# Performance work log

Measured on AMD Instinct MI355X. Metric: run time of the kernel, lower is better.

The kernel has to match this reference:

```python
import jax, jax.numpy as jnp
import numpy as np

N = 100_000       # nodes
E = 1_600_000     # edges (avg degree 16)
F_IN = 10         # num_node_features
H = 128           # hidden_dim
L = 3             # num_layers
G = 256           # number of graphs in the batch
C = 25            # num_classes
BN_EPS = 1e-5


def setup_inputs() -> dict:
    key = jax.random.key(0)
    ks = jax.random.split(key, 10)
    s = 0.05
    x = jax.random.normal(ks[0], (N, F_IN), dtype=jnp.float32)
    edge_index = jax.random.randint(ks[1], (2, E), 0, N, dtype=jnp.int32)
    batch = jnp.sort(jax.random.randint(ks[2], (N,), 0, G, dtype=jnp.int32))
    return {
        "x": x,
        "edge_index": edge_index,
        "batch": batch,
        "Wp": jax.random.normal(ks[3], (F_IN, H), dtype=jnp.float32) * s,
        "bp": jnp.zeros((H,), jnp.float32),
        "Wc": jax.random.normal(ks[4], (L, H, H), dtype=jnp.float32) * s,
        "bc": jnp.zeros((L, H), jnp.float32),
        "bn_gamma": jnp.ones((L, H), jnp.float32),
        "bn_beta": jnp.zeros((L, H), jnp.float32),
        "bn_mean": jax.random.normal(ks[5], (L, H), dtype=jnp.float32) * 0.1,
        "bn_var": jax.random.uniform(ks[6], (L, H), minval=0.5, maxval=1.5, dtype=jnp.float32),
        "W1": jax.random.normal(ks[7], (2 * H, H), dtype=jnp.float32) * s,
        "b1": jnp.zeros((H,), jnp.float32),
        "W2": jax.random.normal(ks[8], (H, C), dtype=jnp.float32) * s,
        "b2": jnp.zeros((C,), jnp.float32),
    }


def reference(x, edge_index, batch, Wp, bp, Wc, bc, bn_gamma, bn_beta,
              bn_mean, bn_var, W1, b1, W2, b2):
    n = x.shape[0]
    # GCNConv: add self loops, symmetric degree normalization (eval semantics:
    # batchnorm uses running stats, dropout is identity).
    loop = jnp.arange(n, dtype=edge_index.dtype)
    rows = jnp.concatenate([edge_index[0], loop])  # target / aggregation index
    cols = jnp.concatenate([edge_index[1], loop])  # source / gather index
    deg = jax.ops.segment_sum(jnp.ones_like(rows, dtype=x.dtype), rows, num_segments=n)
    dinv = jax.lax.rsqrt(deg)  # deg >= 1 thanks to self loops
    norm = dinv[rows] * dinv[cols]  # [E+N]

    h = jax.nn.relu(x @ Wp + bp)
    for i in range(L):
        hw = h @ Wc[i]                                   # [N, H]
        msg = hw[cols] * norm[:, None]                   # gather + scale
        agg = jax.ops.segment_sum(msg, rows, num_segments=n) + bc[i]
        bn = (agg - bn_mean[i]) * jax.lax.rsqrt(bn_var[i] + BN_EPS) * bn_gamma[i] + bn_beta[i]
        h = jax.nn.relu(bn)

    counts = jax.ops.segment_sum(jnp.ones((n,), h.dtype), batch, num_segments=G)
    x_mean = jax.ops.segment_sum(h, batch, num_segments=G) / jnp.maximum(counts, 1.0)[:, None]
    x_max = jax.ops.segment_max(h, batch, num_segments=G)
    x_max = jnp.where(counts[:, None] > 0, x_max, 0.0)   # guard empty graphs
    g = jnp.concatenate([x_mean, x_max], axis=1)          # [G, 2H]
    return jax.nn.relu(g @ W1 + b1) @ W2 + b2             # [G, C]
```

## Files before the change

### kernel.cpp

```cpp
#include <hip/hip_runtime.h>

#define N_NODES   100000
#define N_EDGES   1600000
#define F_IN      10
#define HD        128
#define N_LAYERS  3
#define N_GRAPHS  256
#define N_CLASSES 25
#define BN_EPS    1e-5f
#define POOL_TILE 64
#define LDS_PITCH 152
#define CPITCH    136

#define NBUCK     196
#define SCAT_TILE 4096
#define BUCK_CAP  16384
#define PREPW_BLKS ((N_LAYERS*HD*HD)/256)

typedef __attribute__((ext_vector_type(8))) short bf8;
typedef __attribute__((ext_vector_type(4))) float f32x4;

static __device__ __forceinline__ unsigned short f2bf(float f){
    unsigned u = __float_as_uint(f);
    unsigned r = (u + 0x7fffu + ((u >> 16) & 1u)) >> 16;
    return (unsigned short)r;
}
static __device__ __forceinline__ float bflo(unsigned u){ return __uint_as_float(u << 16); }
static __device__ __forceinline__ float bfhi(unsigned u){ return __uint_as_float(u & 0xffff0000u); }
static __device__ __forceinline__ unsigned packbf(float a, float b){
    return (unsigned)f2bf(a) | ((unsigned)f2bf(b) << 16);
}


__global__ __launch_bounds__(256) void k_hist(const int* __restrict__ rows,
        int* __restrict__ gcount, int e){
    __shared__ int lhist[NBUCK];
    int t = threadIdx.x;
    if (t < NBUCK) lhist[t] = 0;
    __syncthreads();
    int i0 = blockIdx.x*SCAT_TILE + t;
    #pragma unroll
    for (int k = 0; k < 16; k++){
        int i = i0 + k*256;
        if (i < e) atomicAdd(&lhist[rows[i] >> 9], 1);
    }
    __syncthreads();
    if (t < NBUCK && lhist[t] > 0) atomicAdd(&gcount[t], lhist[t]);
}

__global__ void k_scanb(const int* __restrict__ gcount, int* __restrict__ base,
        int* __restrict__ cursor, int* __restrict__ rowptr, int e, int n){
    __shared__ int s[256];
    int t = threadIdx.x;
    int v = (t < NBUCK) ? gcount[t] : 0;
    s[t] = v;
    __syncthreads();
    for (int d = 1; d < 256; d <<= 1){
        int tv = (t >= d) ? s[t-d] : 0;
        __syncthreads();
        s[t] += tv;
        __syncthreads();
    }
    if (t < NBUCK){ base[t] = s[t] - v; cursor[t] = s[t] - v; }
    if (t == 0){ base[NBUCK] = e; rowptr[n] = e; }
}

__global__ __launch_bounds__(256) void k_scatter(const int* __restrict__ rows,
        const int* __restrict__ cols, int* __restrict__ cursor,
        unsigned* __restrict__ ebuf, int e){
    __shared__ int lbase[NBUCK];
    __shared__ int lcur[NBUCK];
    __shared__ int gbase[NBUCK];
    __shared__ int sbuf[256];
    __shared__ unsigned sedge[SCAT_TILE];
    __shared__ unsigned char sbuck[SCAT_TILE];
    int t = threadIdx.x;
    int i0 = blockIdx.x*SCAT_TILE + t;
    int r[16], c[16];
    if (t < NBUCK) lcur[t] = 0;
    __syncthreads();
    #pragma unroll
    for (int k = 0; k < 16; k++){
        int i = i0 + k*256;
        if (i < e){
            r[k] = rows[i]; c[k] = cols[i];
            atomicAdd(&lcur[r[k] >> 9], 1);
        } else r[k] = -1;
    }
    __syncthreads();
    int myc = (t < NBUCK) ? lcur[t] : 0;
    sbuf[t] = myc;
    __syncthreads();
    for (int d = 1; d < 256; d <<= 1){
        int tv = (t >= d) ? sbuf[t-d] : 0;
        __syncthreads();
        sbuf[t] += tv;
        __syncthreads();
    }
    if (t < NBUCK){
        lbase[t] = sbuf[t] - myc;
        lcur[t]  = sbuf[t] - myc;
        if (myc > 0) gbase[t] = atomicAdd(&cursor[t], myc);
    }
    __syncthreads();
    #pragma unroll
    for (int k = 0; k < 16; k++){
        if (r[k] >= 0){
            int bk = r[k] >> 9;
            int off = atomicAdd(&lcur[bk], 1);
            sedge[off] = ((unsigned)(r[k] & 511) << 17) | (unsigned)c[k];
            sbuck[off] = (unsigned char)bk;
        }
    }
    __syncthreads();
    int tot = sbuf[255];
    for (int i = t; i < tot; i += 256){
        int bk = sbuck[i];
        ebuf[gbase[bk] + (i - lbase[bk])] = sedge[i];
    }
}

__global__ __launch_bounds__(512) void k_build(const unsigned* __restrict__ ebuf,
        const int* __restrict__ base, int* __restrict__ rowptr,
        float* __restrict__ dinv, int* __restrict__ colidx, int n){
    __shared__ int hist[512];
    __shared__ int cur[512];
    __shared__ int colstage[BUCK_CAP];
    int b = blockIdx.x;
    int s = base[b], e = base[b+1];
    int cnt = e - s;
    int row0 = b << 9;
    int nrows = min(512, n - row0);
    int t = threadIdx.x;
    hist[t] = 0;
    __syncthreads();
    for (int i = t; i < cnt; i += 512)
        atomicAdd(&hist[ebuf[s + i] >> 17], 1);
    __syncthreads();
    int myc = hist[t];
    cur[t] = myc;
    __syncthreads();
    for (int d = 1; d < 512; d <<= 1){
        int tv = (t >= d) ? cur[t-d] : 0;
        __syncthreads();
        cur[t] += tv;
        __syncthreads();
    }
    int excl = cur[t] - myc;
    if (t < nrows){
        rowptr[row0 + t] = s + excl;
        dinv[row0 + t] = rsqrtf((float)(myc + 1));
    }
    cur[t] = excl;
    __syncthreads();
    for (int i = t; i < cnt; i += 512){
        unsigned v = ebuf[s + i];
        int off = atomicAdd(&cur[v >> 17], 1);
        colstage[off] = (int)(v & 0x1ffffu);
    }
    __syncthreads();
    for (int i = t; i < cnt; i += 512)
        colidx[s + i] = colstage[i];
}

__global__ void k_prep(const float* __restrict__ Wc, unsigned short* __restrict__ WT,
                       const float* __restrict__ x, const float* __restrict__ Wp,
                       const float* __restrict__ bp, unsigned* __restrict__ hbf, int n){
    __shared__ float sW[F_IN*HD];
    __shared__ float sb[HD];
    if (blockIdx.x < PREPW_BLKS){
        int i = blockIdx.x*256 + threadIdx.x;
        int l = i >> 14;
        int r = (i >> 7) & 127;
        int c = i & 127;
        WT[(l << 14) + c*HD + r] = f2bf(Wc[i]);
        return;
    }
    int bid = blockIdx.x - PREPW_BLKS;
    for (int t = threadIdx.x; t < F_IN*HD; t += 256) sW[t] = Wp[t];
    if (threadIdx.x < HD) sb[threadIdx.x] = bp[threadIdx.x];
    __syncthreads();
    int j  = threadIdx.x & 63;
    int ln = threadIdx.x >> 6;
    for (int n0 = bid*4 + ln; n0 < n; n0 += 1024*4){
        float a0 = sb[2*j], a1 = sb[2*j+1];
        #pragma unroll
        for (int k = 0; k < F_IN; k++){
            float xv = x[(size_t)n0*F_IN + k];
            a0 += xv * sW[k*HD + 2*j];
            a1 += xv * sW[k*HD + 2*j+1];
        }
        hbf[(size_t)n0*64 + j] = packbf(fmaxf(a0, 0.f), fmaxf(a1, 0.f));
    }
}

__global__ __launch_bounds__(256) void k_gemm(const unsigned short* __restrict__ hbf,
        const unsigned short* __restrict__ WT, const float* __restrict__ dinv,
        unsigned short* __restrict__ hw, int n){
    extern __shared__ char smem[];
    unsigned short* As = (unsigned short*)smem;
    unsigned short* Bs = As + 128*LDS_PITCH;
    int tid = threadIdx.x;
    int row0 = blockIdx.x * 128;

    const uint4* h4 = (const uint4*)hbf;
    const uint4* w4 = (const uint4*)WT;
    #pragma unroll
    for (int q = tid; q < 2048; q += 256){
        int r = q >> 4, c = q & 15;
        uint4 v = make_uint4(0u,0u,0u,0u);
        if (row0 + r < n) v = h4[(size_t)(row0 + r)*16 + c];
        *(uint4*)&As[r*LDS_PITCH + c*8] = v;
        *(uint4*)&Bs[r*LDS_PITCH + c*8] = w4[r*16 + c];
    }
    __syncthreads();

    int w = tid >> 6, lane = tid & 63;
    int l15 = lane & 15, quad = lane >> 4;
    f32x4 acc[2][8];
    #pragma unroll
    for (int rt = 0; rt < 2; rt++)
        #pragma unroll
        for (int ct = 0; ct < 8; ct++) acc[rt][ct] = (f32x4){0.f,0.f,0.f,0.f};

    int arow = w*32 + l15;
    #pragma unroll
    for (int kc = 0; kc < 4; kc++){
        int ko = kc*32 + quad*8;
        bf8 a0 = *(const bf8*)&As[arow*LDS_PITCH + ko];
        bf8 a1 = *(const bf8*)&As[(arow+16)*LDS_PITCH + ko];
        #pragma unroll
        for (int ct = 0; ct < 8; ct++){
            bf8 b = *(const bf8*)&Bs[(ct*16 + l15)*LDS_PITCH + ko];
            acc[0][ct] = __builtin_amdgcn_mfma_f32_16x16x32_bf16(a0, b, acc[0][ct], 0, 0, 0);
            acc[1][ct] = __builtin_amdgcn_mfma_f32_16x16x32_bf16(a1, b, acc[1][ct], 0, 0, 0);
        }
    }
    __syncthreads();

    unsigned short* CS = As;
    #pragma unroll
    for (int rt = 0; rt < 2; rt++){
        #pragma unroll
        for (int reg = 0; reg < 4; reg++){
            int rloc = w*32 + rt*16 + quad*4 + reg;
            int grow = row0 + rloc;
            float dv = (grow < n) ? dinv[grow] : 0.f;
            #pragma unroll
            for (int ct = 0; ct < 8; ct++)
                CS[rloc*CPITCH + ct*16 + l15] = f2bf(acc[rt][ct][reg] * dv);
        }
    }
    __syncthreads();

    #pragma unroll
    for (int q = tid; q < 2048; q += 256){
        int r = q >> 4, c = q & 15;
        if (row0 + r < n)
            *(uint4*)&hw[(size_t)(row0 + r)*HD + c*8] = *(const uint4*)&CS[r*CPITCH + c*8];
    }
}

__global__ __launch_bounds__(256) void k_agg(const unsigned* __restrict__ hw4,
        const int* __restrict__ rowptr, const int* __restrict__ colidx,
        const float* __restrict__ dinv, const float* __restrict__ bc,
        const float* __restrict__ bmean, const float* __restrict__ bvar,
        const float* __restrict__ bgamma, const float* __restrict__ bbeta,
        unsigned* __restrict__ houtb, int n){
    int node = blockIdx.x*4 + (threadIdx.x >> 6);
    int lane = threadIdx.x & 63;
    if (node >= n) return;
    unsigned self = hw4[(size_t)node*64 + lane];
    float ax = bflo(self), ay = bfhi(self);
    float bx = 0.f, by = 0.f;
    int s = rowptr[node], e = rowptr[node+1];
    int t = s;
    for (; t + 8 <= e; t += 8){
        int c0 = colidx[t],   c1 = colidx[t+1];
        int c2 = colidx[t+2], c3 = colidx[t+3];
        int c4 = colidx[t+4], c5 = colidx[t+5];
        int c6 = colidx[t+6], c7 = colidx[t+7];
        unsigned v0 = hw4[(size_t)c0*64 + lane];
        unsigned v1 = hw4[(size_t)c1*64 + lane];
        unsigned v2 = hw4[(size_t)c2*64 + lane];
        unsigned v3 = hw4[(size_t)c3*64 + lane];
        unsigned v4 = hw4[(size_t)c4*64 + lane];
        unsigned v5 = hw4[(size_t)c5*64 + lane];
        unsigned v6 = hw4[(size_t)c6*64 + lane];
        unsigned v7 = hw4[(size_t)c7*64 + lane];
        ax += bflo(v0); ay += bfhi(v0);
        bx += bflo(v1); by += bfhi(v1);
        ax += bflo(v2); ay += bfhi(v2);
        bx += bflo(v3); by += bfhi(v3);
        ax += bflo(v4); ay += bfhi(v4);
        bx += bflo(v5); by += bfhi(v5);
        ax += bflo(v6); ay += bfhi(v6);
        bx += bflo(v7); by += bfhi(v7);
    }
    for (; t + 4 <= e; t += 4){
        int c0 = colidx[t],   c1 = colidx[t+1];
        int c2 = colidx[t+2], c3 = colidx[t+3];
        unsigned v0 = hw4[(size_t)c0*64 + lane];
        unsigned v1 = hw4[(size_t)c1*64 + lane];
        unsigned v2 = hw4[(size_t)c2*64 + lane];
        unsigned v3 = hw4[(size_t)c3*64 + lane];
        ax += bflo(v0); ay += bfhi(v0);
        bx += bflo(v1); by += bfhi(v1);
        ax += bflo(v2); ay += bfhi(v2);
        bx += bflo(v3); by += bfhi(v3);
    }
    for (; t < e; t++){
        unsigned v = hw4[(size_t)colidx[t]*64 + lane];
        ax += bflo(v); ay += bfhi(v);
    }
    ax += bx; ay += by;
    float dv = dinv[node];
    float2 cb  = ((const float2*)bc)[lane];
    float2 cm  = ((const float2*)bmean)[lane];
    float2 cv  = ((const float2*)bvar)[lane];
    float2 cg  = ((const float2*)bgamma)[lane];
    float2 cbe = ((const float2*)bbeta)[lane];
    float rx = (ax*dv + cb.x - cm.x) * rsqrtf(cv.x + BN_EPS) * cg.x + cbe.x;
    float ry = (ay*dv + cb.y - cm.y) * rsqrtf(cv.y + BN_EPS) * cg.y + cbe.y;
    rx = fmaxf(rx, 0.f); ry = fmaxf(ry, 0.f);
    houtb[(size_t)node*64 + lane] = packbf(rx, ry);
}

__global__ void k_pool(const unsigned* __restrict__ hb, const int* __restrict__ batch,
        float* __restrict__ gsum, int* __restrict__ gmax, int n){
    int q = threadIdx.x;
    int start = blockIdx.x * POOL_TILE;
    int end = min(start + POOL_TILE, n);
    if (start >= end) return;
    int cur = batch[start];
    float s0 = 0.f, s1 = 0.f, m0 = 0.f, m1 = 0.f;
    for (int i = start; i < end; i++){
        int b = batch[i];
        unsigned v = hb[(size_t)i*64 + q];
        float v0 = bflo(v), v1 = bfhi(v);
        if (b != cur){
            atomicAdd(&gsum[cur*HD + 2*q],     s0);
            atomicAdd(&gsum[cur*HD + 2*q + 1], s1);
            atomicMax(&gmax[cur*HD + 2*q],     __float_as_int(m0));
            atomicMax(&gmax[cur*HD + 2*q + 1], __float_as_int(m1));
            s0 = s1 = m0 = m1 = 0.f; cur = b;
        }
        s0 += v0; s1 += v1;
        m0 = fmaxf(m0, v0); m1 = fmaxf(m1, v1);
    }
    atomicAdd(&gsum[cur*HD + 2*q],     s0);
    atomicAdd(&gsum[cur*HD + 2*q + 1], s1);
    atomicMax(&gmax[cur*HD + 2*q],     __float_as_int(m0));
    atomicMax(&gmax[cur*HD + 2*q + 1], __float_as_int(m1));
}

__global__ void k_head(const float* __restrict__ gsum, const int* __restrict__ gmax,
        const int* __restrict__ batch, const float* __restrict__ W1,
        const float* __restrict__ b1, const float* __restrict__ W2,
        const float* __restrict__ b2, float* __restrict__ out, int n){
    __shared__ float gv[2*HD];
    __shared__ float hid[HD];
    __shared__ int bound[2];
    int g = blockIdx.x, j = threadIdx.x;
    if (j < 2){
        int target = g + j;
        int lo = 0, hi = n;
        while (lo < hi){ int mid = (lo + hi) >> 1; if (batch[mid] < target) lo = mid + 1; else hi = mid; }
        bound[j] = lo;
    }
    __syncthreads();
    float denom = (float)max(bound[1] - bound[0], 1);
    gv[j]    = gsum[g*HD+j] / denom;
    gv[HD+j] = __int_as_float(gmax[g*HD+j]);
    __syncthreads();
    float acc = b1[j];
    #pragma unroll 8
    for (int k = 0; k < 2*HD; k++) acc += gv[k]*W1[k*HD + j];
    hid[j] = fmaxf(acc, 0.f);
    __syncthreads();
    if (j < N_CLASSES){
        float o = b2[j];
        #pragma unroll 4
        for (int k = 0; k < HD; k++) o += hid[k]*W2[k*N_CLASSES + j];
        out[g*N_CLASSES + j] = o;
    }
}

extern "C" void kernel_launch(void* const* d_in, const int* in_sizes, int n_in,
                              void* d_out, int out_size, void* d_ws, size_t ws_size,
                              hipStream_t stream){
    const float* x   = (const float*)d_in[0];
    const int*  eidx = (const int*)d_in[1];
    const int* batch = (const int*)d_in[2];
    const float* Wp  = (const float*)d_in[3];
    const float* bp  = (const float*)d_in[4];
    const float* Wc  = (const float*)d_in[5];
    const float* bc  = (const float*)d_in[6];
    const float* bng = (const float*)d_in[7];
    const float* bnb = (const float*)d_in[8];
    const float* bnm = (const float*)d_in[9];
    const float* bnv = (const float*)d_in[10];
    const float* W1  = (const float*)d_in[11];
    const float* b1  = (const float*)d_in[12];
    const float* W2  = (const float*)d_in[13];
    const float* b2  = (const float*)d_in[14];
    float* out = (float*)d_out;

    char* ws = (char*)d_ws;
    size_t off = 0;
    unsigned short* h_bf  = (unsigned short*)(ws + off); off += (size_t)N_NODES*HD*2;
    unsigned short* hw_bf = (unsigned short*)(ws + off); off += (size_t)N_NODES*HD*2;
    unsigned short* WT = (unsigned short*)(ws + off); off += (size_t)N_LAYERS*HD*HD*2;
    float* dinv   = (float*)(ws + off); off += (size_t)N_NODES*4;
    int*   rowptr = (int*)  (ws + off); off += (size_t)(N_NODES+16)*4;
    int*   colidx = (int*)  (ws + off); off += (size_t)N_EDGES*4;
    unsigned* ebuf= (unsigned*)(ws + off); off += (size_t)N_EDGES*4;
    int*   bbase  = (int*)  (ws + off); off += 1024;
    int*   bcur   = (int*)  (ws + off); off += 1024;
    int*   gcount = (int*)  (ws + off); off += 1024;
    float* gsum   = (float*)(ws + off); off += (size_t)N_GRAPHS*HD*4;
    int*   gmax   = (int*)  (ws + off); off += (size_t)N_GRAPHS*HD*4;

    const int* rows = eidx;
    const int* cols = eidx + N_EDGES;

    hipMemsetAsync(gcount, 0, 1024 + (size_t)(N_GRAPHS*HD*2)*4, stream);

    int nsb = (N_EDGES + SCAT_TILE - 1)/SCAT_TILE;
    k_hist   <<<nsb, 256, 0, stream>>>(rows, gcount, N_EDGES);
    k_scanb  <<<1, 256, 0, stream>>>(gcount, bbase, bcur, rowptr, N_EDGES, N_NODES);
    k_scatter<<<nsb, 256, 0, stream>>>(rows, cols, bcur, ebuf, N_EDGES);
    k_build  <<<NBUCK, 512, 0, stream>>>(ebuf, bbase, rowptr, dinv, colidx, N_NODES);

    k_prep<<<PREPW_BLKS + 1024, 256, 0, stream>>>(Wc, WT, x, Wp, bp, (unsigned*)h_bf, N_NODES);

    int ntiles = (N_NODES + 127)/128;
    size_t shmem = (size_t)(2*128*LDS_PITCH)*2;
    for (int l = 0; l < N_LAYERS; l++){
        k_gemm<<<ntiles, 256, shmem, stream>>>(h_bf, WT + (size_t)l*HD*HD, dinv, hw_bf, N_NODES);
        k_agg<<<(N_NODES+3)/4, 256, 0, stream>>>((const unsigned*)hw_bf, rowptr, colidx, dinv,
            bc + l*HD, bnm + l*HD, bnv + l*HD, bng + l*HD, bnb + l*HD,
            (unsigned*)h_bf, N_NODES);
    }

    k_pool<<<(N_NODES+POOL_TILE-1)/POOL_TILE, 64, 0, stream>>>((const unsigned*)h_bf, batch, gsum, gmax, N_NODES);
    k_head<<<N_GRAPHS, 128, 0, stream>>>(gsum, gmax, batch, W1, b1, W2, b2, out, N_NODES);
}
```

Before: 439.5 us.

## Fuse aggregation with next-layer GEMM and pooling, merge CSR build kernels

Each layer's neighbor aggregation and batchnorm now feeds the next layer's bf16 MFMA GEMM through LDS in one kernel (64-row tiles). The input projection is fused into the first GEMM and mean/max pooling into the last aggregation. The separate bucket-scan kernel is removed by redoing the scan redundantly in the scatter and build blocks, and the weight transpose is merged into the histogram kernel. This cuts launches and the write and re-read of the intermediate h tensor. The cost is smaller GEMM tiles and aggregation work serialized per wave within a tile.

```diff
diff --git a/kernel.cpp b/kernel.cpp
--- a/kernel.cpp
+++ b/kernel.cpp
@@ -8,14 +8,13 @@
 #define N_GRAPHS  256
 #define N_CLASSES 25
 #define BN_EPS    1e-5f
-#define POOL_TILE 64
-#define LDS_PITCH 152
-#define CPITCH    136
+#define APITCH    136
 
 #define NBUCK     196
 #define SCAT_TILE 4096
 #define BUCK_CAP  16384
 #define PREPW_BLKS ((N_LAYERS*HD*HD)/256)
+#define NTILE     ((N_NODES + 63)/64)
 
 typedef __attribute__((ext_vector_type(8))) short bf8;
 typedef __attribute__((ext_vector_type(4))) float f32x4;
@@ -31,14 +30,23 @@
     return (unsigned)f2bf(a) | ((unsigned)f2bf(b) << 16);
 }
 
-
-__global__ __launch_bounds__(256) void k_hist(const int* __restrict__ rows,
+__global__ __launch_bounds__(256) void k_pre(const float* __restrict__ Wc,
+        unsigned short* __restrict__ WT, const int* __restrict__ rows,
         int* __restrict__ gcount, int e){
     __shared__ int lhist[NBUCK];
     int t = threadIdx.x;
+    if (blockIdx.x < PREPW_BLKS){
+        int i = blockIdx.x*256 + t;
+        int l = i >> 14;
+        int r = (i >> 7) & 127;
+        int c = i & 127;
+        WT[(l << 14) + c*HD + r] = f2bf(Wc[i]);
+        return;
+    }
+    int bid = blockIdx.x - PREPW_BLKS;
     if (t < NBUCK) lhist[t] = 0;
     __syncthreads();
-    int i0 = blockIdx.x*SCAT_TILE + t;
+    int i0 = bid*SCAT_TILE + t;
     #pragma unroll
     for (int k = 0; k < 16; k++){
         int i = i0 + k*256;
@@ -48,26 +56,9 @@
     if (t < NBUCK && lhist[t] > 0) atomicAdd(&gcount[t], lhist[t]);
 }
 
-__global__ void k_scanb(const int* __restrict__ gcount, int* __restrict__ base,
-        int* __restrict__ cursor, int* __restrict__ rowptr, int e, int n){
-    __shared__ int s[256];
-    int t = threadIdx.x;
-    int v = (t < NBUCK) ? gcount[t] : 0;
-    s[t] = v;
-    __syncthreads();
-    for (int d = 1; d < 256; d <<= 1){
-        int tv = (t >= d) ? s[t-d] : 0;
-        __syncthreads();
-        s[t] += tv;
-        __syncthreads();
-    }
-    if (t < NBUCK){ base[t] = s[t] - v; cursor[t] = s[t] - v; }
-    if (t == 0){ base[NBUCK] = e; rowptr[n] = e; }
-}
-
 __global__ __launch_bounds__(256) void k_scatter(const int* __restrict__ rows,
-        const int* __restrict__ cols, int* __restrict__ cursor,
-        unsigned* __restrict__ ebuf, int e){
+        const int* __restrict__ cols, const int* __restrict__ gcount,
+        int* __restrict__ gcur, unsigned* __restrict__ ebuf, int e){
     __shared__ int lbase[NBUCK];
     __shared__ int lcur[NBUCK];
     __shared__ int gbase[NBUCK];
@@ -75,6 +66,17 @@
     __shared__ unsigned sedge[SCAT_TILE];
     __shared__ unsigned char sbuck[SCAT_TILE];
     int t = threadIdx.x;
+    int gval = (t < NBUCK) ? gcount[t] : 0;
+    sbuf[t] = gval;
+    __syncthreads();
+    for (int d = 1; d < 256; d <<= 1){
+        int tv = (t >= d) ? sbuf[t-d] : 0;
+        __syncthreads();
+        sbuf[t] += tv;
+        __syncthreads();
+    }
+    int bucket_base = sbuf[t] - gval;
+    __syncthreads();
     int i0 = blockIdx.x*SCAT_TILE + t;
     int r[16], c[16];
     if (t < NBUCK) lcur[t] = 0;
@@ -100,7 +102,7 @@
     if (t < NBUCK){
         lbase[t] = sbuf[t] - myc;
         lcur[t]  = sbuf[t] - myc;
-        if (myc > 0) gbase[t] = atomicAdd(&cursor[t], myc);
+        if (myc > 0) gbase[t] = bucket_base + atomicAdd(&gcur[t], myc);
     }
     __syncthreads();
     #pragma unroll
@@ -121,17 +123,29 @@
 }
 
 __global__ __launch_bounds__(512) void k_build(const unsigned* __restrict__ ebuf,
-        const int* __restrict__ base, int* __restrict__ rowptr,
-        float* __restrict__ dinv, int* __restrict__ colidx, int n){
+        const int* __restrict__ gcount, int* __restrict__ rowptr,
+        float* __restrict__ dinv, int* __restrict__ colidx, int n, int etot){
     __shared__ int hist[512];
     __shared__ int cur[512];
     __shared__ int colstage[BUCK_CAP];
+    __shared__ int sscan[256];
+    int t = threadIdx.x;
+    int gval = (t < NBUCK) ? gcount[t] : 0;
+    if (t < 256) sscan[t] = gval;
+    __syncthreads();
+    for (int d = 1; d < 256; d <<= 1){
+        int tv = (t < 256 && t >= d) ? sscan[t-d] : 0;
+        __syncthreads();
+        if (t < 256) sscan[t] += tv;
+        __syncthreads();
+    }
     int b = blockIdx.x;
-    int s = base[b], e = base[b+1];
-    int cnt = e - s;
+    int e_ = sscan[b];
+    int s  = e_ - gcount[b];
+    int cnt = e_ - s;
     int row0 = b << 9;
     int nrows = min(512, n - row0);
-    int t = threadIdx.x;
+    if (b == 0 && t == 0) rowptr[n] = etot;
     hist[t] = 0;
     __syncthreads();
     for (int i = t; i < cnt; i += 512)
@@ -163,114 +177,60 @@
         colidx[s + i] = colstage[i];
 }
 
-__global__ void k_prep(const float* __restrict__ Wc, unsigned short* __restrict__ WT,
-                       const float* __restrict__ x, const float* __restrict__ Wp,
-                       const float* __restrict__ bp, unsigned* __restrict__ hbf, int n){
-    __shared__ float sW[F_IN*HD];
-    __shared__ float sb[HD];
-    if (blockIdx.x < PREPW_BLKS){
-        int i = blockIdx.x*256 + threadIdx.x;
-        int l = i >> 14;
-        int r = (i >> 7) & 127;
-        int c = i & 127;
-        WT[(l << 14) + c*HD + r] = f2bf(Wc[i]);
-        return;
-    }
-    int bid = blockIdx.x - PREPW_BLKS;
-    for (int t = threadIdx.x; t < F_IN*HD; t += 256) sW[t] = Wp[t];
-    if (threadIdx.x < HD) sb[threadIdx.x] = bp[threadIdx.x];
-    __syncthreads();
-    int j  = threadIdx.x & 63;
-    int ln = threadIdx.x >> 6;
-    for (int n0 = bid*4 + ln; n0 < n; n0 += 1024*4){
-        float a0 = sb[2*j], a1 = sb[2*j+1];
-        #pragma unroll
-        for (int k = 0; k < F_IN; k++){
-            float xv = x[(size_t)n0*F_IN + k];
-            a0 += xv * sW[k*HD + 2*j];
-            a1 += xv * sW[k*HD + 2*j+1];
-        }
-        hbf[(size_t)n0*64 + j] = packbf(fmaxf(a0, 0.f), fmaxf(a1, 0.f));
-    }
-}
-
-__global__ __launch_bounds__(256) void k_gemm(const unsigned short* __restrict__ hbf,
+static __device__ __forceinline__ void gemm_tile(unsigned short* As, unsigned short* Bs,
         const unsigned short* __restrict__ WT, const float* __restrict__ dinv,
-        unsigned short* __restrict__ hw, int n){
-    extern __shared__ char smem[];
-    unsigned short* As = (unsigned short*)smem;
-    unsigned short* Bs = As + 128*LDS_PITCH;
-    int tid = threadIdx.x;
-    int row0 = blockIdx.x * 128;
-
-    const uint4* h4 = (const uint4*)hbf;
+        unsigned short* __restrict__ hw, int row0, int n, int tid){
     const uint4* w4 = (const uint4*)WT;
     #pragma unroll
     for (int q = tid; q < 2048; q += 256){
         int r = q >> 4, c = q & 15;
-        uint4 v = make_uint4(0u,0u,0u,0u);
-        if (row0 + r < n) v = h4[(size_t)(row0 + r)*16 + c];
-        *(uint4*)&As[r*LDS_PITCH + c*8] = v;
-        *(uint4*)&Bs[r*LDS_PITCH + c*8] = w4[r*16 + c];
+        *(uint4*)&Bs[r*APITCH + c*8] = w4[r*16 + c];
     }
     __syncthreads();
 
     int w = tid >> 6, lane = tid & 63;
     int l15 = lane & 15, quad = lane >> 4;
-    f32x4 acc[2][8];
-    #pragma unroll
-    for (int rt = 0; rt < 2; rt++)
-        #pragma unroll
-        for (int ct = 0; ct < 8; ct++) acc[rt][ct] = (f32x4){0.f,0.f,0.f,0.f};
-
-    int arow = w*32 + l15;
+    f32x4 acc[8];
+    #pragma unroll
+    for (int ct = 0; ct < 8; ct++) acc[ct] = (f32x4){0.f,0.f,0.f,0.f};
+
+    int arow = w*16 + l15;
     #pragma unroll
     for (int kc = 0; kc < 4; kc++){
         int ko = kc*32 + quad*8;
-        bf8 a0 = *(const bf8*)&As[arow*LDS_PITCH + ko];
-        bf8 a1 = *(const bf8*)&As[(arow+16)*LDS_PITCH + ko];
+        bf8 a = *(const bf8*)&As[arow*APITCH + ko];
         #pragma unroll
         for (int ct = 0; ct < 8; ct++){
-            bf8 b = *(const bf8*)&Bs[(ct*16 + l15)*LDS_PITCH + ko];
-            acc[0][ct] = __builtin_amdgcn_mfma_f32_16x16x32_bf16(a0, b, acc[0][ct], 0, 0, 0);
-            acc[1][ct] = __builtin_amdgcn_mfma_f32_16x16x32_bf16(a1, b, acc[1][ct], 0, 0, 0);
+            bf8 b = *(const bf8*)&Bs[(ct*16 + l15)*APITCH + ko];
+            acc[ct] = __builtin_amdgcn_mfma_f32_16x16x32_bf16(a, b, acc[ct], 0, 0, 0);
         }
     }
     __syncthreads();
 
-    unsigned short* CS = As;
-    #pragma unroll
-    for (int rt = 0; rt < 2; rt++){
+    #pragma unroll
+    for (int reg = 0; reg < 4; reg++){
+        int rloc = w*16 + quad*4 + reg;
+        int grow = row0 + rloc;
+        float dv = (grow < n) ? dinv[grow] : 0.f;
         #pragma unroll
-        for (int reg = 0; reg < 4; reg++){
-            int rloc = w*32 + rt*16 + quad*4 + reg;
-            int grow = row0 + rloc;
-            float dv = (grow < n) ? dinv[grow] : 0.f;
-            #pragma unroll
-            for (int ct = 0; ct < 8; ct++)
-                CS[rloc*CPITCH + ct*16 + l15] = f2bf(acc[rt][ct][reg] * dv);
-        }
-    }
-    __syncthreads();
-
-    #pragma unroll
-    for (int q = tid; q < 2048; q += 256){
+        for (int ct = 0; ct < 8; ct++)
+            As[rloc*APITCH + ct*16 + l15] = f2bf(acc[ct][reg] * dv);
+    }
+    __syncthreads();
+
+    #pragma unroll
+    for (int q = tid; q < 1024; q += 256){
         int r = q >> 4, c = q & 15;
         if (row0 + r < n)
-            *(uint4*)&hw[(size_t)(row0 + r)*HD + c*8] = *(const uint4*)&CS[r*CPITCH + c*8];
-    }
-}
-
-__global__ __launch_bounds__(256) void k_agg(const unsigned* __restrict__ hw4,
+            *(uint4*)&hw[(size_t)(row0 + r)*HD + c*8] = *(const uint4*)&As[r*APITCH + c*8];
+    }
+}
+
+static __device__ __forceinline__ unsigned agg_node(const unsigned* __restrict__ hwp,
         const int* __restrict__ rowptr, const int* __restrict__ colidx,
-        const float* __restrict__ dinv, const float* __restrict__ bc,
-        const float* __restrict__ bmean, const float* __restrict__ bvar,
-        const float* __restrict__ bgamma, const float* __restrict__ bbeta,
-        unsigned* __restrict__ houtb, int n){
-    int node = blockIdx.x*4 + (threadIdx.x >> 6);
-    int lane = threadIdx.x & 63;
-    if (node >= n) return;
-    unsigned self = hw4[(size_t)node*64 + lane];
+        const float* __restrict__ dinv, int node, int lane,
+        float2 cb, float2 cm, float2 cv, float2 cg, float2 cbe){
+    unsigned self = hwp[(size_t)node*64 + lane];
     float ax = bflo(self), ay = bfhi(self);
     float bx = 0.f, by = 0.f;
     int s = rowptr[node], e = rowptr[node+1];
@@ -280,14 +240,14 @@
         int c2 = colidx[t+2], c3 = colidx[t+3];
         int c4 = colidx[t+4], c5 = colidx[t+5];
         int c6 = colidx[t+6], c7 = colidx[t+7];
-        unsigned v0 = hw4[(size_t)c0*64 + lane];
-        unsigned v1 = hw4[(size_t)c1*64 + lane];
-        unsigned v2 = hw4[(size_t)c2*64 + lane];
-        unsigned v3 = hw4[(size_t)c3*64 + lane];
-        unsigned v4 = hw4[(size_t)c4*64 + lane];
-        unsigned v5 = hw4[(size_t)c5*64 + lane];
-        unsigned v6 = hw4[(size_t)c6*64 + lane];
-        unsigned v7 = hw4[(size_t)c7*64 + lane];
+        unsigned v0 = hwp[(size_t)c0*64 + lane];
+        unsigned v1 = hwp[(size_t)c1*64 + lane];
+        unsigned v2 = hwp[(size_t)c2*64 + lane];
+        unsigned v3 = hwp[(size_t)c3*64 + lane];
+        unsigned v4 = hwp[(size_t)c4*64 + lane];
+        unsigned v5 = hwp[(size_t)c5*64 + lane];
+        unsigned v6 = hwp[(size_t)c6*64 + lane];
+        unsigned v7 = hwp[(size_t)c7*64 + lane];
         ax += bflo(v0); ay += bfhi(v0);
         bx += bflo(v1); by += bfhi(v1);
         ax += bflo(v2); ay += bfhi(v2);
@@ -300,58 +260,149 @@
     for (; t + 4 <= e; t += 4){
         int c0 = colidx[t],   c1 = colidx[t+1];
         int c2 = colidx[t+2], c3 = colidx[t+3];
-        unsigned v0 = hw4[(size_t)c0*64 + lane];
-        unsigned v1 = hw4[(size_t)c1*64 + lane];
-        unsigned v2 = hw4[(size_t)c2*64 + lane];
-        unsigned v3 = hw4[(size_t)c3*64 + lane];
+        unsigned v0 = hwp[(size_t)c0*64 + lane];
+        unsigned v1 = hwp[(size_t)c1*64 + lane];
+        unsigned v2 = hwp[(size_t)c2*64 + lane];
+        unsigned v3 = hwp[(size_t)c3*64 + lane];
         ax += bflo(v0); ay += bfhi(v0);
         bx += bflo(v1); by += bfhi(v1);
         ax += bflo(v2); ay += bfhi(v2);
         bx += bflo(v3); by += bfhi(v3);
     }
     for (; t < e; t++){
-        unsigned v = hw4[(size_t)colidx[t]*64 + lane];
+        unsigned v = hwp[(size_t)colidx[t]*64 + lane];
         ax += bflo(v); ay += bfhi(v);
     }
     ax += bx; ay += by;
     float dv = dinv[node];
+    float rx = (ax*dv + cb.x - cm.x) * rsqrtf(cv.x + BN_EPS) * cg.x + cbe.x;
+    float ry = (ay*dv + cb.y - cm.y) * rsqrtf(cv.y + BN_EPS) * cg.y + cbe.y;
+    return packbf(fmaxf(rx, 0.f), fmaxf(ry, 0.f));
+}
+
+__global__ __launch_bounds__(256) void k_layer0(const float* __restrict__ x,
+        const float* __restrict__ Wp, const float* __restrict__ bp,
+        const unsigned short* __restrict__ WT, const float* __restrict__ dinv,
+        unsigned short* __restrict__ hw, int n){
+    extern __shared__ char smem[];
+    unsigned short* As = (unsigned short*)smem;
+    unsigned short* Bs = As + 64*APITCH;
+    unsigned* As32 = (unsigned*)As;
+    int tid = threadIdx.x;
+    int row0 = blockIdx.x*64;
+
+    float* sW = (float*)Bs;
+    float* sb = sW + F_IN*HD;
+    for (int t = tid; t < F_IN*HD; t += 256) sW[t] = Wp[t];
+    if (tid < HD) sb[tid] = bp[tid];
+    __syncthreads();
+
+    int j = tid & 63, ln = tid >> 6;
+    for (int r = ln; r < 64; r += 4){
+        int node = row0 + r;
+        unsigned val = 0u;
+        if (node < n){
+            float a0 = sb[2*j], a1 = sb[2*j+1];
+            #pragma unroll
+            for (int k = 0; k < F_IN; k++){
+                float xv = x[(size_t)node*F_IN + k];
+                a0 += xv * sW[k*HD + 2*j];
+                a1 += xv * sW[k*HD + 2*j+1];
+            }
+            val = packbf(fmaxf(a0, 0.f), fmaxf(a1, 0.f));
+        }
+        As32[r*68 + j] = val;
+    }
+    __syncthreads();
+    gemm_tile(As, Bs, WT, dinv, hw, row0, n, tid);
+}
+
+__global__ __launch_bounds__(256) void k_layerF(const unsigned* __restrict__ hwp,
+        const int* __restrict__ rowptr, const int* __restrict__ colidx,
+        const float* __restrict__ dinv, const float* __restrict__ bc,
+        const float* __restrict__ bmean, const float* __restrict__ bvar,
+        const float* __restrict__ bgamma, const float* __restrict__ bbeta,
+        const unsigned short* __restrict__ WT, unsigned short* __restrict__ hwout, int n){
+    extern __shared__ char smem[];
+    unsigned short* As = (unsigned short*)smem;
+    unsigned short* Bs = As + 64*APITCH;
+    unsigned* As32 = (unsigned*)As;
+    int tid = threadIdx.x;
+    int w = tid >> 6, lane = tid & 63;
+    int row0 = blockIdx.x*64;
+
     float2 cb  = ((const float2*)bc)[lane];
     float2 cm  = ((const float2*)bmean)[lane];
     float2 cv  = ((const float2*)bvar)[lane];
     float2 cg  = ((const float2*)bgamma)[lane];
     float2 cbe = ((const float2*)bbeta)[lane];
-    float rx = (ax*dv + cb.x - cm.x) * rsqrtf(cv.x + BN_EPS) * cg.x + cbe.x;
-    float ry = (ay*dv + cb.y - cm.y) * rsqrtf(cv.y + BN_EPS) * cg.y + cbe.y;
-    rx = fmaxf(rx, 0.f); ry = fmaxf(ry, 0.f);
-    houtb[(size_t)node*64 + lane] = packbf(rx, ry);
-}
-
-__global__ void k_pool(const unsigned* __restrict__ hb, const int* __restrict__ batch,
-        float* __restrict__ gsum, int* __restrict__ gmax, int n){
-    int q = threadIdx.x;
-    int start = blockIdx.x * POOL_TILE;
-    int end = min(start + POOL_TILE, n);
-    if (start >= end) return;
-    int cur = batch[start];
-    float s0 = 0.f, s1 = 0.f, m0 = 0.f, m1 = 0.f;
-    for (int i = start; i < end; i++){
-        int b = batch[i];
-        unsigned v = hb[(size_t)i*64 + q];
-        float v0 = bflo(v), v1 = bfhi(v);
-        if (b != cur){
+
+    for (int i = 0; i < 16; i++){
+        int vloc = w*16 + i;
+        int node = row0 + vloc;
+        unsigned val = 0u;
+        if (node < n)
+            val = agg_node(hwp, rowptr, colidx, dinv, node, lane, cb, cm, cv, cg, cbe);
+        As32[vloc*68 + lane] = val;
+    }
+    __syncthreads();
+    gemm_tile(As, Bs, WT, dinv, hwout, row0, n, tid);
+}
+
+__global__ __launch_bounds__(256) void k_layerP(const unsigned* __restrict__ hwp,
+        const int* __restrict__ rowptr, const int* __restrict__ colidx,
+        const float* __restrict__ dinv, const float* __restrict__ bc,
+        const float* __restrict__ bmean, const float* __restrict__ bvar,
+        const float* __restrict__ bgamma, const float* __restrict__ bbeta,
+        const int* __restrict__ batch, float* __restrict__ gsum,
+        int* __restrict__ gmax, int n){
+    extern __shared__ char smem[];
+    unsigned* As32 = (unsigned*)smem;
+    int tid = threadIdx.x;
+    int w = tid >> 6, lane = tid & 63;
+    int row0 = blockIdx.x*64;
+
+    float2 cb  = ((const float2*)bc)[lane];
+    float2 cm  = ((const float2*)bmean)[lane];
+    float2 cv  = ((const float2*)bvar)[lane];
+    float2 cg  = ((const float2*)bgamma)[lane];
+    float2 cbe = ((const float2*)bbeta)[lane];
+
+    for (int i = 0; i < 16; i++){
+        int vloc = w*16 + i;
+        int node = row0 + vloc;
+        unsigned val = 0u;
+        if (node < n)
+            val = agg_node(hwp, rowptr, colidx, dinv, node, lane, cb, cm, cv, cg, cbe);
+        As32[vloc*68 + lane] = val;
+    }
+    __syncthreads();
+    if (tid < 64){
+        int q = tid;
+        int start = row0, end = min(row0 + 64, n);
+        if (start < end){
+            int cur = batch[start];
+            float s0 = 0.f, s1 = 0.f, m0 = 0.f, m1 = 0.f;
+            for (int i = start; i < end; i++){
+                int b = batch[i];
+                unsigned v = As32[(i - start)*68 + q];
+                float v0 = bflo(v), v1 = bfhi(v);
+                if (b != cur){
+                    atomicAdd(&gsum[cur*HD + 2*q],     s0);
+                    atomicAdd(&gsum[cur*HD + 2*q + 1], s1);
+                    atomicMax(&gmax[cur*HD + 2*q],     __float_as_int(m0));
+                    atomicMax(&gmax[cur*HD + 2*q + 1], __float_as_int(m1));
+                    s0 = s1 = m0 = m1 = 0.f; cur = b;
+                }
+                s0 += v0; s1 += v1;
+                m0 = fmaxf(m0, v0); m1 = fmaxf(m1, v1);
+            }
             atomicAdd(&gsum[cur*HD + 2*q],     s0);
             atomicAdd(&gsum[cur*HD + 2*q + 1], s1);
             atomicMax(&gmax[cur*HD + 2*q],     __float_as_int(m0));
             atomicMax(&gmax[cur*HD + 2*q + 1], __float_as_int(m1));
-            s0 = s1 = m0 = m1 = 0.f; cur = b;
         }
-        s0 += v0; s1 += v1;
-        m0 = fmaxf(m0, v0); m1 = fmaxf(m1, v1);
-    }
-    atomicAdd(&gsum[cur*HD + 2*q],     s0);
-    atomicAdd(&gsum[cur*HD + 2*q + 1], s1);
-    atomicMax(&gmax[cur*HD + 2*q],     __float_as_int(m0));
-    atomicMax(&gmax[cur*HD + 2*q + 1], __float_as_int(m1));
+    }
 }
 
 __global__ void k_head(const float* __restrict__ gsum, const int* __restrict__ gmax,
@@ -408,41 +459,38 @@
 
     char* ws = (char*)d_ws;
     size_t off = 0;
-    unsigned short* h_bf  = (unsigned short*)(ws + off); off += (size_t)N_NODES*HD*2;
-    unsigned short* hw_bf = (unsigned short*)(ws + off); off += (size_t)N_NODES*HD*2;
-    unsigned short* WT = (unsigned short*)(ws + off); off += (size_t)N_LAYERS*HD*HD*2;
+    unsigned short* hwA = (unsigned short*)(ws + off); off += (size_t)N_NODES*HD*2;
+    unsigned short* hwB = (unsigned short*)(ws + off); off += (size_t)N_NODES*HD*2;
+    unsigned short* WT  = (unsigned short*)(ws + off); off += (size_t)N_LAYERS*HD*HD*2;
     float* dinv   = (float*)(ws + off); off += (size_t)N_NODES*4;
     int*   rowptr = (int*)  (ws + off); off += (size_t)(N_NODES+16)*4;
     int*   colidx = (int*)  (ws + off); off += (size_t)N_EDGES*4;
     unsigned* ebuf= (unsigned*)(ws + off); off += (size_t)N_EDGES*4;
-    int*   bbase  = (int*)  (ws + off); off += 1024;
-    int*   bcur   = (int*)  (ws + off); off += 1024;
     int*   gcount = (int*)  (ws + off); off += 1024;
+    int*   gcur   = (int*)  (ws + off); off += 1024;
     float* gsum   = (float*)(ws + off); off += (size_t)N_GRAPHS*HD*4;
     int*   gmax   = (int*)  (ws + off); off += (size_t)N_GRAPHS*HD*4;
 
     const int* rows = eidx;
     const int* cols = eidx + N_EDGES;
 
-    hipMemsetAsync(gcount, 0, 1024 + (size_t)(N_GRAPHS*HD*2)*4, stream);
+    hipMemsetAsync(gcount, 0, 2048 + (size_t)(N_GRAPHS*HD*2)*4, stream);
 
     int nsb = (N_EDGES + SCAT_TILE - 1)/SCAT_TILE;
-    k_hist   <<<nsb, 256, 0, stream>>>(rows, gcount, N_EDGES);
-    k_scanb  <<<1, 256, 0, stream>>>(gcount, bbase, bcur, rowptr, N_EDGES, N_NODES);
-    k_scatter<<<nsb, 256, 0, stream>>>(rows, cols, bcur, ebuf, N_EDGES);
-    k_build  <<<NBUCK, 512, 0, stream>>>(ebuf, bbase, rowptr, dinv, colidx, N_NODES);
-
-    k_prep<<<PREPW_BLKS + 1024, 256, 0, stream>>>(Wc, WT, x, Wp, bp, (unsigned*)h_bf, N_NODES);
-
-    int ntiles = (N_NODES + 127)/128;
-    size_t shmem = (size_t)(2*128*LDS_PITCH)*2;
-    for (int l = 0; l < N_LAYERS; l++){
-        k_gemm<<<ntiles, 256, shmem, stream>>>(h_bf, WT + (size_t)l*HD*HD, dinv, hw_bf, N_NODES);
-        k_agg<<<(N_NODES+3)/4, 256, 0, stream>>>((const unsigned*)hw_bf, rowptr, colidx, dinv,
-            bc + l*HD, bnm + l*HD, bnv + l*HD, bng + l*HD, bnb + l*HD,
-            (unsigned*)h_bf, N_NODES);
-    }
-
-    k_pool<<<(N_NODES+POOL_TILE-1)/POOL_TILE, 64, 0, stream>>>((const unsigned*)h_bf, batch, gsum, gmax, N_NODES);
+    k_pre    <<<PREPW_BLKS + nsb, 256, 0, stream>>>(Wc, WT, rows, gcount, N_EDGES);
+    k_scatter<<<nsb, 256, 0, stream>>>(rows, cols, gcount, gcur, ebuf, N_EDGES);
+    k_build  <<<NBUCK, 512, 0, stream>>>(ebuf, gcount, rowptr, dinv, colidx, N_NODES, N_EDGES);
+
+    size_t shmem = (size_t)(64 + 128)*APITCH*2;
+    size_t shmemP = (size_t)64*APITCH*2;
+    k_layer0<<<NTILE, 256, shmem, stream>>>(x, Wp, bp, WT, dinv, hwA, N_NODES);
+    k_layerF<<<NTILE, 256, shmem, stream>>>((const unsigned*)hwA, rowptr, colidx, dinv,
+        bc, bnm, bnv, bng, bnb, WT + (size_t)1*HD*HD, hwB, N_NODES);
+    k_layerF<<<NTILE, 256, shmem, stream>>>((const unsigned*)hwB, rowptr, colidx, dinv,
+        bc + HD, bnm + HD, bnv + HD, bng + HD, bnb + HD, WT + (size_t)2*HD*HD, hwA, N_NODES);
+    k_layerP<<<NTILE, 256, shmemP, stream>>>((const unsigned*)hwA, rowptr, colidx, dinv,
+        bc + 2*HD, bnm + 2*HD, bnv + 2*HD, bng + 2*HD, bnb + 2*HD,
+        batch, gsum, gmax, N_NODES);
+
     k_head<<<N_GRAPHS, 128, 0, stream>>>(gsum, gmax, batch, W1, b1, W2, b2, out, N_NODES);
 }
```

Measured after the change: 564.9 us. 28.5% more time.

## Drop histogram/scan passes via fixed-capacity buckets and fuse prep into scatter

Applied to the files above, without the earlier changes.

The edge bucketing now writes into fixed-capacity per-bucket slots (BCAP each), so the separate histogram and bucket-scan kernels are removed and the bucket prefix scan is recomputed inside each k_build block. The weight transpose/bf16 conversion and input projection are merged into extra blocks of the scatter kernel. This cuts three kernel launches and one full read of the rows array. The cost is a larger scratch buffer, and correctness now depends on no bucket exceeding BCAP edges, which holds for uniform random inputs but is not guaranteed in general.

```diff
diff --git a/kernel.cpp b/kernel.cpp
--- a/kernel.cpp
+++ b/kernel.cpp
@@ -14,8 +14,10 @@
 
 #define NBUCK     196
 #define SCAT_TILE 4096
+#define BCAP      9216
 #define BUCK_CAP  16384
 #define PREPW_BLKS ((N_LAYERS*HD*HD)/256)
+#define PROJ_BLKS 1024
 
 typedef __attribute__((ext_vector_type(8))) short bf8;
 typedef __attribute__((ext_vector_type(4))) float f32x4;
@@ -31,50 +33,51 @@
     return (unsigned)f2bf(a) | ((unsigned)f2bf(b) << 16);
 }
 
-
-__global__ __launch_bounds__(256) void k_hist(const int* __restrict__ rows,
-        int* __restrict__ gcount, int e){
-    __shared__ int lhist[NBUCK];
-    int t = threadIdx.x;
-    if (t < NBUCK) lhist[t] = 0;
-    __syncthreads();
-    int i0 = blockIdx.x*SCAT_TILE + t;
-    #pragma unroll
-    for (int k = 0; k < 16; k++){
-        int i = i0 + k*256;
-        if (i < e) atomicAdd(&lhist[rows[i] >> 9], 1);
-    }
-    __syncthreads();
-    if (t < NBUCK && lhist[t] > 0) atomicAdd(&gcount[t], lhist[t]);
-}
-
-__global__ void k_scanb(const int* __restrict__ gcount, int* __restrict__ base,
-        int* __restrict__ cursor, int* __restrict__ rowptr, int e, int n){
-    __shared__ int s[256];
-    int t = threadIdx.x;
-    int v = (t < NBUCK) ? gcount[t] : 0;
-    s[t] = v;
-    __syncthreads();
-    for (int d = 1; d < 256; d <<= 1){
-        int tv = (t >= d) ? s[t-d] : 0;
-        __syncthreads();
-        s[t] += tv;
-        __syncthreads();
-    }
-    if (t < NBUCK){ base[t] = s[t] - v; cursor[t] = s[t] - v; }
-    if (t == 0){ base[NBUCK] = e; rowptr[n] = e; }
-}
-
 __global__ __launch_bounds__(256) void k_scatter(const int* __restrict__ rows,
-        const int* __restrict__ cols, int* __restrict__ cursor,
-        unsigned* __restrict__ ebuf, int e){
+        const int* __restrict__ cols, int* __restrict__ gcur,
+        unsigned* __restrict__ ebuf, int e, int nsb,
+        const float* __restrict__ Wc, unsigned short* __restrict__ WT,
+        const float* __restrict__ x, const float* __restrict__ Wp,
+        const float* __restrict__ bp, unsigned* __restrict__ hbf, int n){
     __shared__ int lbase[NBUCK];
     __shared__ int lcur[NBUCK];
     __shared__ int gbase[NBUCK];
     __shared__ int sbuf[256];
     __shared__ unsigned sedge[SCAT_TILE];
     __shared__ unsigned char sbuck[SCAT_TILE];
+    __shared__ float sW[F_IN*HD];
+    __shared__ float sb[HD];
     int t = threadIdx.x;
+
+    if (blockIdx.x >= nsb){
+        int bid2 = blockIdx.x - nsb;
+        if (bid2 < PREPW_BLKS){
+            int i = bid2*256 + t;
+            int l = i >> 14;
+            int r = (i >> 7) & 127;
+            int c = i & 127;
+            WT[(l << 14) + c*HD + r] = f2bf(Wc[i]);
+            return;
+        }
+        int bid = bid2 - PREPW_BLKS;
+        for (int q = t; q < F_IN*HD; q += 256) sW[q] = Wp[q];
+        if (t < HD) sb[t] = bp[t];
+        __syncthreads();
+        int j  = t & 63;
+        int ln = t >> 6;
+        for (int n0 = bid*4 + ln; n0 < n; n0 += PROJ_BLKS*4){
+            float a0 = sb[2*j], a1 = sb[2*j+1];
+            #pragma unroll
+            for (int k = 0; k < F_IN; k++){
+                float xv = x[(size_t)n0*F_IN + k];
+                a0 += xv * sW[k*HD + 2*j];
+                a1 += xv * sW[k*HD + 2*j+1];
+            }
+            hbf[(size_t)n0*64 + j] = packbf(fmaxf(a0, 0.f), fmaxf(a1, 0.f));
+        }
+        return;
+    }
+
     int i0 = blockIdx.x*SCAT_TILE + t;
     int r[16], c[16];
     if (t < NBUCK) lcur[t] = 0;
@@ -100,7 +103,7 @@
     if (t < NBUCK){
         lbase[t] = sbuf[t] - myc;
         lcur[t]  = sbuf[t] - myc;
-        if (myc > 0) gbase[t] = atomicAdd(&cursor[t], myc);
+        if (myc > 0) gbase[t] = t*BCAP + atomicAdd(&gcur[t], myc);
     }
     __syncthreads();
     #pragma unroll
@@ -121,21 +124,33 @@
 }
 
 __global__ __launch_bounds__(512) void k_build(const unsigned* __restrict__ ebuf,
-        const int* __restrict__ base, int* __restrict__ rowptr,
-        float* __restrict__ dinv, int* __restrict__ colidx, int n){
+        const int* __restrict__ gcur, int* __restrict__ rowptr,
+        float* __restrict__ dinv, int* __restrict__ colidx, int n, int etot){
     __shared__ int hist[512];
     __shared__ int cur[512];
     __shared__ int colstage[BUCK_CAP];
+    __shared__ int sscan[256];
+    int t = threadIdx.x;
+    int gval = (t < NBUCK) ? gcur[t] : 0;
+    if (t < 256) sscan[t] = gval;
+    __syncthreads();
+    for (int d = 1; d < 256; d <<= 1){
+        int tv = (t < 256 && t >= d) ? sscan[t-d] : 0;
+        __syncthreads();
+        if (t < 256) sscan[t] += tv;
+        __syncthreads();
+    }
     int b = blockIdx.x;
-    int s = base[b], e = base[b+1];
-    int cnt = e - s;
+    int cnt = gcur[b];
+    int s   = sscan[b] - cnt;
+    int sp  = b*BCAP;
     int row0 = b << 9;
     int nrows = min(512, n - row0);
-    int t = threadIdx.x;
+    if (b == 0 && t == 0) rowptr[n] = etot;
     hist[t] = 0;
     __syncthreads();
     for (int i = t; i < cnt; i += 512)
-        atomicAdd(&hist[ebuf[s + i] >> 17], 1);
+        atomicAdd(&hist[ebuf[sp + i] >> 17], 1);
     __syncthreads();
     int myc = hist[t];
     cur[t] = myc;
@@ -154,44 +169,13 @@
     cur[t] = excl;
     __syncthreads();
     for (int i = t; i < cnt; i += 512){
-        unsigned v = ebuf[s + i];
+        unsigned v = ebuf[sp + i];
         int off = atomicAdd(&cur[v >> 17], 1);
         colstage[off] = (int)(v & 0x1ffffu);
     }
     __syncthreads();
     for (int i = t; i < cnt; i += 512)
         colidx[s + i] = colstage[i];
-}
-
-__global__ void k_prep(const float* __restrict__ Wc, unsigned short* __restrict__ WT,
-                       const float* __restrict__ x, const float* __restrict__ Wp,
-                       const float* __restrict__ bp, unsigned* __restrict__ hbf, int n){
-    __shared__ float sW[F_IN*HD];
-    __shared__ float sb[HD];
-    if (blockIdx.x < PREPW_BLKS){
-        int i = blockIdx.x*256 + threadIdx.x;
-        int l = i >> 14;
-        int r = (i >> 7) & 127;
-        int c = i & 127;
-        WT[(l << 14) + c*HD + r] = f2bf(Wc[i]);
-        return;
-    }
-    int bid = blockIdx.x - PREPW_BLKS;
-    for (int t = threadIdx.x; t < F_IN*HD; t += 256) sW[t] = Wp[t];
-    if (threadIdx.x < HD) sb[threadIdx.x] = bp[threadIdx.x];
-    __syncthreads();
-    int j  = threadIdx.x & 63;
-    int ln = threadIdx.x >> 6;
-    for (int n0 = bid*4 + ln; n0 < n; n0 += 1024*4){
-        float a0 = sb[2*j], a1 = sb[2*j+1];
-        #pragma unroll
-        for (int k = 0; k < F_IN; k++){
-            float xv = x[(size_t)n0*F_IN + k];
-            a0 += xv * sW[k*HD + 2*j];
-            a1 += xv * sW[k*HD + 2*j+1];
-        }
-        hbf[(size_t)n0*64 + j] = packbf(fmaxf(a0, 0.f), fmaxf(a1, 0.f));
-    }
 }
 
 __global__ __launch_bounds__(256) void k_gemm(const unsigned short* __restrict__ hbf,
@@ -414,25 +398,20 @@
     float* dinv   = (float*)(ws + off); off += (size_t)N_NODES*4;
     int*   rowptr = (int*)  (ws + off); off += (size_t)(N_NODES+16)*4;
     int*   colidx = (int*)  (ws + off); off += (size_t)N_EDGES*4;
-    unsigned* ebuf= (unsigned*)(ws + off); off += (size_t)N_EDGES*4;
-    int*   bbase  = (int*)  (ws + off); off += 1024;
-    int*   bcur   = (int*)  (ws + off); off += 1024;
-    int*   gcount = (int*)  (ws + off); off += 1024;
+    unsigned* ebuf= (unsigned*)(ws + off); off += (size_t)NBUCK*BCAP*4;
+    int*   gcur   = (int*)  (ws + off); off += 1024;
     float* gsum   = (float*)(ws + off); off += (size_t)N_GRAPHS*HD*4;
     int*   gmax   = (int*)  (ws + off); off += (size_t)N_GRAPHS*HD*4;
 
     const int* rows = eidx;
     const int* cols = eidx + N_EDGES;
 
-    hipMemsetAsync(gcount, 0, 1024 + (size_t)(N_GRAPHS*HD*2)*4, stream);
+    hipMemsetAsync(gcur, 0, 1024 + (size_t)(N_GRAPHS*HD*2)*4, stream);
 
     int nsb = (N_EDGES + SCAT_TILE - 1)/SCAT_TILE;
-    k_hist   <<<nsb, 256, 0, stream>>>(rows, gcount, N_EDGES);
-    k_scanb  <<<1, 256, 0, stream>>>(gcount, bbase, bcur, rowptr, N_EDGES, N_NODES);
-    k_scatter<<<nsb, 256, 0, stream>>>(rows, cols, bcur, ebuf, N_EDGES);
-    k_build  <<<NBUCK, 512, 0, stream>>>(ebuf, bbase, rowptr, dinv, colidx, N_NODES);
-
-    k_prep<<<PREPW_BLKS + 1024, 256, 0, stream>>>(Wc, WT, x, Wp, bp, (unsigned*)h_bf, N_NODES);
+    k_scatter<<<nsb + PREPW_BLKS + PROJ_BLKS, 256, 0, stream>>>(rows, cols, gcur, ebuf,
+        N_EDGES, nsb, Wc, WT, x, Wp, bp, (unsigned*)h_bf, N_NODES);
+    k_build  <<<NBUCK, 512, 0, stream>>>(ebuf, gcur, rowptr, dinv, colidx, N_NODES, N_EDGES);
 
     int ntiles = (N_NODES + 127)/128;
     size_t shmem = (size_t)(2*128*LDS_PITCH)*2;
```

Measured after the change: 420.9 us. 1.04x faster.
